# Optimization experiments

Hardware: AMD Instinct MI355X
Metric: run time of the kernel (lower is better)

## Reference

```python
import jax, jax.numpy as jnp
import numpy as np


def setup_inputs() -> dict:
    key = jax.random.key(0)
    k1, k2 = jax.random.split(key)
    B, N, M, D = 8, 8192, 8192, 3
    gts = jax.random.normal(k1, (B, N, D), dtype=jnp.float32)
    preds = jax.random.normal(k2, (B, M, D), dtype=jnp.float32)
    return {"gts": gts, "preds": preds}


def reference(gts, preds):
    # Chamfer distance (pytorch3d defaults): squared L2, mean over points,
    # mean over batch, sum of both directions.
    x2 = jnp.sum(gts * gts, axis=-1)          # [B, N]
    y2 = jnp.sum(preds * preds, axis=-1)      # [B, M]
    xy = jnp.einsum('bnd,bmd->bnm', gts, preds)  # [B, N, M]
    d2 = x2[:, :, None] + y2[:, None, :] - 2.0 * xy
    d2 = jnp.maximum(d2, 0.0)  # guard tiny negative values from cancellation
    cham_x = jnp.mean(jnp.min(d2, axis=2))  # x -> nearest y, mean over N then B
    cham_y = jnp.mean(jnp.min(d2, axis=1))  # y -> nearest x, mean over M then B
    return cham_x + cham_y
```

## Files before the change

### kernel.cpp

```cpp
#include <hip/hip_runtime.h>
#include <hip/hip_bf16.h>
#include <math.h>


#define BLOCK 256
#define WAVES 4
#define QPW 64
#define NCHUNK 2

typedef short short8 __attribute__((ext_vector_type(8)));
typedef float f32x16 __attribute__((ext_vector_type(16)));

union U16S { uint4 v; short8 s; };

__device__ __forceinline__ unsigned int bf16hi(float f) {
    __hip_bfloat16 h = __float2bfloat16(f);
    return (unsigned int)*reinterpret_cast<unsigned short*>(&h);
}
__device__ __forceinline__ float bf16f(unsigned int u) {
    unsigned short us = (unsigned short)u;
    __hip_bfloat16 h;
    *reinterpret_cast<unsigned short*>(&h) = us;
    return __bfloat162float(h);
}

__device__ __forceinline__ f32x16 mfma_bf16(short8 a, short8 b, f32x16 c) {
    f32x16 d;
    asm volatile("v_mfma_f32_32x32x16_bf16 %0, %1, %2, %3"
                 : "=v"(d) : "v"(a), "v"(b), "v"(c));
    return d;
}
__device__ __forceinline__ void mfma_fence4(f32x16& a, f32x16& b, f32x16& c, f32x16& d) {
    asm volatile("s_nop 7\n\ts_nop 7" : "+v"(a), "+v"(b), "+v"(c), "+v"(d));
}

__global__ void prep_kernel(const float* __restrict__ gts, const float* __restrict__ preds,
                            int nG, int nP, uint4* __restrict__ recG, uint4* __restrict__ recP,
                            float* out) {
    const int idx = blockIdx.x * blockDim.x + threadIdx.x;
    if (idx == 0) out[0] = 0.0f;
    if (idx >= nG + nP) return;
    const float* src;
    uint4* dst;
    if (idx < nG) { src = gts + 3 * (size_t)idx;          dst = recG + idx; }
    else          { src = preds + 3 * (size_t)(idx - nG); dst = recP + (idx - nG); }
    const float x = src[0], y = src[1], z = src[2];
    const float w = -0.5f * (x * x + y * y + z * z);
    const unsigned int xh = bf16hi(x), yh = bf16hi(y), zh = bf16hi(z), wh = bf16hi(w);
    const unsigned int xl = bf16hi(x - bf16f(xh));
    const unsigned int yl = bf16hi(y - bf16f(yh));
    const unsigned int zl = bf16hi(z - bf16f(zh));
    const unsigned int wl = bf16hi(w - bf16f(wh));
    *dst = make_uint4(xh | (yh << 16), zh | (wh << 16),
                      xl | (yl << 16), zl | (wl << 16));
}

__global__ void __launch_bounds__(BLOCK, 4)
nn_kernel(const uint4* __restrict__ recG, const uint4* __restrict__ recP,
          float* __restrict__ kpart, int N, int M, int B) {
    const int z = blockIdx.z;
    const bool dirX = (z < B);
    const int b = dirX ? z : z - B;
    const int NQ = dirX ? N : M;
    const int NR = dirX ? M : N;
    const uint4* Qr = (dirX ? recG : recP) + (size_t)b * NQ;
    const uint4* Rr = (dirX ? recP : recG) + (size_t)b * NR;
    const int nGP = B * (N + M) / 2 * 2;
    float* outK = kpart + (size_t)blockIdx.y * nGP + (dirX ? 0 : B * N) + (size_t)b * NQ;

    const int tid = threadIdx.x;
    const int lane = tid & 63;
    const int wave = tid >> 6;
    const int m = lane & 31;
    const bool hiK = lane >= 32;
    const unsigned int loMask = hiK ? 0u : 0xFFFFFFFFu;
    const int qBase = (blockIdx.x * WAVES + wave) * QPW;

    const uint4 q0 = Qr[qBase + m];
    const uint4 q1 = Qr[qBase + 32 + m];
    U16S a;
    a.v.x = q0.x;
    a.v.y = (q0.y & 0xFFFFu) | 0x3F800000u;
    a.v.z = q0.z & loMask;
    a.v.w = q0.w & 0xFFFFu & loMask;
    const short8 A0 = a.s;
    a.v.x = q1.x;
    a.v.y = (q1.y & 0xFFFFu) | 0x3F800000u;
    a.v.z = q1.z & loMask;
    a.v.w = q1.w & 0xFFFFu & loMask;
    const short8 A1 = a.s;

    f32x16 zc;
    #pragma unroll
    for (int r = 0; r < 16; ++r) zc[r] = 0.0f;
    f32x16 k0, k1;
    #pragma unroll
    for (int r = 0; r < 16; ++r) { k0[r] = -INFINITY; k1[r] = -INFINITY; }

    const int chunk = NR / NCHUNK;
    const uint2* p = (const uint2*)(Rr + (size_t)blockIdx.y * chunk) + 2 * m + (hiK ? 1 : 0);
    const int iters = chunk / 64;

    uint2 t0 = p[0], t1 = p[64];
    #pragma unroll 1
    for (int it = 0; it < iters; ++it) {
        const uint2 n0 = p[128];
        const uint2 n1 = p[192];

        U16S b0, b1;
        b0.v.x = t0.x;          b0.v.y = t0.y;
        b0.v.z = t0.x & loMask; b0.v.w = t0.y & loMask;
        b1.v.x = t1.x;          b1.v.y = t1.y;
        b1.v.z = t1.x & loMask; b1.v.w = t1.y & loMask;

        f32x16 c0 = mfma_bf16(A0, b0.s, zc);
        f32x16 c1 = mfma_bf16(A1, b0.s, zc);
        f32x16 c2 = mfma_bf16(A0, b1.s, zc);
        f32x16 c3 = mfma_bf16(A1, b1.s, zc);
        mfma_fence4(c0, c1, c2, c3);
        #pragma unroll
        for (int r = 0; r < 16; ++r) {
            k0[r] = fmaxf(fmaxf(c0[r], c2[r]), k0[r]);
            k1[r] = fmaxf(fmaxf(c1[r], c3[r]), k1[r]);
        }

        t0 = n0; t1 = n1;
        p += 128;
    }

    __shared__ float sT[WAVES][64][36];
    #pragma unroll
    for (int r = 0; r < 16; ++r) {
        const int row = (r & 3) + 8 * (r >> 2) + 4 * (lane >> 5);
        sT[wave][row][m]      = k0[r];
        sT[wave][32 + row][m] = k1[r];
    }
    const float4* rowp = (const float4*)&sT[wave][lane][0];
    float4 m01 = rowp[0];
    #pragma unroll
    for (int kk = 1; kk < 8; ++kk) {
        const float4 t = rowp[kk];
        m01.x = fmaxf(m01.x, t.x); m01.y = fmaxf(m01.y, t.y);
        m01.z = fmaxf(m01.z, t.z); m01.w = fmaxf(m01.w, t.w);
    }
    const float cmax = fmaxf(fmaxf(m01.x, m01.y), fmaxf(m01.z, m01.w));
    outK[qBase + lane] = cmax;
}

__global__ void __launch_bounds__(BLOCK)
reduce_kernel(const float* __restrict__ kpart, const float* __restrict__ gts, int nG,
              const float* __restrict__ preds, int nP,
              float invx, float invy, float* __restrict__ out) {
    const int total = nG + nP;
    float local = 0.0f;
    for (int idx = blockIdx.x * blockDim.x + threadIdx.x; idx < total;
         idx += gridDim.x * blockDim.x) {
        const float c = fmaxf(kpart[idx], kpart[total + idx]);
        const float* q;
        float inv;
        if (idx < nG) { q = gts + 3 * (size_t)idx;          inv = invx; }
        else          { q = preds + 3 * (size_t)(idx - nG); inv = invy; }
        const float q2 = q[0] * q[0] + q[1] * q[1] + q[2] * q[2];
        local += fmaxf(q2 - 2.0f * c, 0.0f) * inv;
    }
    __shared__ float waveSums[BLOCK / 64];
    float v = local;
    #pragma unroll
    for (int off = 32; off; off >>= 1) v += __shfl_xor(v, off);
    if ((threadIdx.x & 63) == 0) waveSums[threadIdx.x >> 6] = v;
    __syncthreads();
    if (threadIdx.x == 0) {
        float s = 0.0f;
        #pragma unroll
        for (int w = 0; w < BLOCK / 64; ++w) s += waveSums[w];
        atomicAdd(out, s);
    }
}

extern "C" void kernel_launch(void* const* d_in, const int* in_sizes, int n_in,
                              void* d_out, int out_size, void* d_ws, size_t ws_size,
                              hipStream_t stream) {
    const float* gts   = (const float*)d_in[0];
    const float* preds = (const float*)d_in[1];
    float* out = (float*)d_out;

    const int B = 8;
    const int N = in_sizes[0] / (B * 3);
    const int M = in_sizes[1] / (B * 3);
    const int nG = B * N, nP = B * M;

    uint4* recG  = (uint4*)d_ws;
    uint4* recP  = recG + nG;
    float* kpart = (float*)(recP + nP);

    prep_kernel<<<(nG + nP + BLOCK - 1) / BLOCK, BLOCK, 0, stream>>>(
        gts, preds, nG, nP, recG, recP, out);

    dim3 grid(N / (WAVES * QPW), NCHUNK, 2 * B);
    nn_kernel<<<grid, BLOCK, 0, stream>>>(recG, recP, kpart, N, M, B);

    reduce_kernel<<<256, BLOCK, 0, stream>>>(
        kpart, gts, nG, preds, nP, 1.0f / (float)nG, 1.0f / (float)nP, out);
}
```

Measured before the change: 97.74 us.

## Stage reference points into LDS via async global_load_lds with double buffering

The reference points are now copied into shared memory in double-buffered stages of 1024 points using direct global-to-LDS loads. The inner loop reads its operands from LDS instead of global memory. To allow plain contiguous copies, prep writes an extra pre-swizzled copy of the reference records plus precomputed squared norms, and reduce reads those norms. The MFMA/max sequence is split into two halves with shorter fences so the max work overlaps the remaining MFMA. The cost is extra workspace, extra prep writes, and a __syncthreads per stage.

```diff
diff --git a/kernel.cpp b/kernel.cpp
--- a/kernel.cpp
+++ b/kernel.cpp
@@ -7,9 +7,15 @@
 #define WAVES 4
 #define QPW 64
 #define NCHUNK 2
+#define SREF 1024
+#define STAGE_BYTES (SREF * 16)
+#define IPS (SREF / 64)
 
 typedef short short8 __attribute__((ext_vector_type(8)));
 typedef float f32x16 __attribute__((ext_vector_type(16)));
+typedef unsigned int u32;
+typedef __attribute__((address_space(1))) const u32 gu32;
+typedef __attribute__((address_space(3))) u32 lu32;
 
 union U16S { uint4 v; short8 s; };
 
@@ -30,42 +36,62 @@
                  : "=v"(d) : "v"(a), "v"(b), "v"(c));
     return d;
 }
-__device__ __forceinline__ void mfma_fence4(f32x16& a, f32x16& b, f32x16& c, f32x16& d) {
-    asm volatile("s_nop 7\n\ts_nop 7" : "+v"(a), "+v"(b), "+v"(c), "+v"(d));
+__device__ __forceinline__ void mfma_fence3(f32x16& a, f32x16& b, f32x16& c) {
+    asm volatile("s_nop 7\n\ts_nop 7" : "+v"(a), "+v"(b), "+v"(c));
+}
+__device__ __forceinline__ void mfma_fence2(f32x16& a, f32x16& b) {
+    asm volatile("s_nop 7\n\ts_nop 7\n\ts_nop 7" : "+v"(a), "+v"(b));
+}
+
+__device__ __forceinline__ void gload_lds16(const void* g, void* l) {
+    __builtin_amdgcn_global_load_lds((gu32*)g, (lu32*)l, 16, 0, 0);
 }
 
 __global__ void prep_kernel(const float* __restrict__ gts, const float* __restrict__ preds,
-                            int nG, int nP, uint4* __restrict__ recG, uint4* __restrict__ recP,
+                            int nG, int nP, uint4* __restrict__ recQ,
+                            unsigned char* __restrict__ recB, float* __restrict__ q2,
                             float* out) {
     const int idx = blockIdx.x * blockDim.x + threadIdx.x;
     if (idx == 0) out[0] = 0.0f;
     if (idx >= nG + nP) return;
     const float* src;
-    uint4* dst;
-    if (idx < nG) { src = gts + 3 * (size_t)idx;          dst = recG + idx; }
-    else          { src = preds + 3 * (size_t)(idx - nG); dst = recP + (idx - nG); }
+    unsigned char* rb;
+    if (idx < nG) {
+        src = gts + 3 * (size_t)idx;
+        rb  = recB + (size_t)(idx >> 5) * 512 + (size_t)(idx & 31) * 8;
+    } else {
+        const int j = idx - nG;
+        src = preds + 3 * (size_t)j;
+        rb  = recB + (size_t)nG * 16 + (size_t)(j >> 5) * 512 + (size_t)(j & 31) * 8;
+    }
     const float x = src[0], y = src[1], z = src[2];
-    const float w = -0.5f * (x * x + y * y + z * z);
+    const float n2 = x * x + y * y + z * z;
+    const float w = -0.5f * n2;
+    q2[idx] = n2;
     const unsigned int xh = bf16hi(x), yh = bf16hi(y), zh = bf16hi(z), wh = bf16hi(w);
     const unsigned int xl = bf16hi(x - bf16f(xh));
     const unsigned int yl = bf16hi(y - bf16f(yh));
     const unsigned int zl = bf16hi(z - bf16f(zh));
     const unsigned int wl = bf16hi(w - bf16f(wh));
-    *dst = make_uint4(xh | (yh << 16), zh | (wh << 16),
-                      xl | (yl << 16), zl | (wl << 16));
+    recQ[idx] = make_uint4(xh | (yh << 16), zh | (wh << 16),
+                           xl | (yl << 16), zl | (wl << 16));
+    *(uint2*)(rb)       = make_uint2(xh | (yh << 16), zh | (wh << 16));
+    *(uint2*)(rb + 256) = make_uint2(xl | (yl << 16), zl | (wl << 16));
 }
 
 __global__ void __launch_bounds__(BLOCK, 4)
-nn_kernel(const uint4* __restrict__ recG, const uint4* __restrict__ recP,
+nn_kernel(const uint4* __restrict__ recQ, const unsigned char* __restrict__ recB,
           float* __restrict__ kpart, int N, int M, int B) {
     const int z = blockIdx.z;
     const bool dirX = (z < B);
     const int b = dirX ? z : z - B;
     const int NQ = dirX ? N : M;
     const int NR = dirX ? M : N;
-    const uint4* Qr = (dirX ? recG : recP) + (size_t)b * NQ;
-    const uint4* Rr = (dirX ? recP : recG) + (size_t)b * NR;
-    const int nGP = B * (N + M) / 2 * 2;
+    const uint4* Qr = recQ + (dirX ? 0 : (size_t)B * N) + (size_t)b * NQ;
+    const int chunk = NR / NCHUNK;
+    const unsigned char* Rb = recB + (dirX ? (size_t)B * N * 16 : 0)
+                              + ((size_t)b * NR + (size_t)blockIdx.y * chunk) * 16;
+    const int nGP = B * (N + M);
     float* outK = kpart + (size_t)blockIdx.y * nGP + (dirX ? 0 : B * N) + (size_t)b * NQ;
 
     const int tid = threadIdx.x;
@@ -97,38 +123,57 @@
     #pragma unroll
     for (int r = 0; r < 16; ++r) { k0[r] = -INFINITY; k1[r] = -INFINITY; }
 
-    const int chunk = NR / NCHUNK;
-    const uint2* p = (const uint2*)(Rr + (size_t)blockIdx.y * chunk) + 2 * m + (hiK ? 1 : 0);
-    const int iters = chunk / 64;
-
-    uint2 t0 = p[0], t1 = p[64];
+    __shared__ __align__(16) unsigned char smem[WAVES * 64 * 36 * 4];
+
+    const unsigned char* gsrc = Rb + (size_t)wave * 4096 + (size_t)lane * 16;
+    unsigned char* lbase = smem + wave * 4096;
+    auto stage_issue = [&](int s) {
+        const unsigned char* g = gsrc + (size_t)s * STAGE_BYTES;
+        unsigned char* l = lbase + ((s & 1) * STAGE_BYTES);
+        #pragma unroll
+        for (int k2 = 0; k2 < 4; ++k2)
+            gload_lds16(g + k2 * 1024, l + k2 * 1024);
+    };
+
+    const int nStages = chunk / SREF;
+    stage_issue(0);
+    __syncthreads();
+
     #pragma unroll 1
-    for (int it = 0; it < iters; ++it) {
-        const uint2 n0 = p[128];
-        const uint2 n1 = p[192];
-
-        U16S b0, b1;
-        b0.v.x = t0.x;          b0.v.y = t0.y;
-        b0.v.z = t0.x & loMask; b0.v.w = t0.y & loMask;
-        b1.v.x = t1.x;          b1.v.y = t1.y;
-        b1.v.z = t1.x & loMask; b1.v.w = t1.y & loMask;
-
-        f32x16 c0 = mfma_bf16(A0, b0.s, zc);
-        f32x16 c1 = mfma_bf16(A1, b0.s, zc);
-        f32x16 c2 = mfma_bf16(A0, b1.s, zc);
-        f32x16 c3 = mfma_bf16(A1, b1.s, zc);
-        mfma_fence4(c0, c1, c2, c3);
+    for (int s = 0; s < nStages; ++s) {
+        if (s + 1 < nStages) stage_issue(s + 1);
+        const uint2* tp = (const uint2*)(smem + ((s & 1) * STAGE_BYTES)) + lane;
+        uint2 t0 = tp[0], t1 = tp[64];
         #pragma unroll
-        for (int r = 0; r < 16; ++r) {
-            k0[r] = fmaxf(fmaxf(c0[r], c2[r]), k0[r]);
-            k1[r] = fmaxf(fmaxf(c1[r], c3[r]), k1[r]);
+        for (int i = 0; i < IPS; ++i) {
+            uint2 n0 = t0, n1 = t1;
+            if (i + 1 < IPS) { n0 = tp[(i + 1) * 128]; n1 = tp[(i + 1) * 128 + 64]; }
+
+            U16S b0, b1;
+            b0.v.x = t0.x;          b0.v.y = t0.y;
+            b0.v.z = t0.x & loMask; b0.v.w = t0.y & loMask;
+            b1.v.x = t1.x;          b1.v.y = t1.y;
+            b1.v.z = t1.x & loMask; b1.v.w = t1.y & loMask;
+
+            f32x16 c0 = mfma_bf16(A0, b0.s, zc);
+            f32x16 c1 = mfma_bf16(A0, b1.s, zc);
+            f32x16 c2 = mfma_bf16(A1, b0.s, zc);
+            mfma_fence3(c0, c1, c2);
+            #pragma unroll
+            for (int r = 0; r < 16; ++r)
+                k0[r] = fmaxf(fmaxf(c0[r], c1[r]), k0[r]);
+            f32x16 c3 = mfma_bf16(A1, b1.s, zc);
+            mfma_fence2(c2, c3);
+            #pragma unroll
+            for (int r = 0; r < 16; ++r)
+                k1[r] = fmaxf(fmaxf(c2[r], c3[r]), k1[r]);
+
+            t0 = n0; t1 = n1;
         }
-
-        t0 = n0; t1 = n1;
-        p += 128;
-    }
-
-    __shared__ float sT[WAVES][64][36];
+        __syncthreads();
+    }
+
+    float (*sT)[64][36] = (float (*)[64][36])smem;
     #pragma unroll
     for (int r = 0; r < 16; ++r) {
         const int row = (r & 3) + 8 * (r >> 2) + 4 * (lane >> 5);
@@ -148,20 +193,15 @@
 }
 
 __global__ void __launch_bounds__(BLOCK)
-reduce_kernel(const float* __restrict__ kpart, const float* __restrict__ gts, int nG,
-              const float* __restrict__ preds, int nP,
-              float invx, float invy, float* __restrict__ out) {
+reduce_kernel(const float* __restrict__ kpart, const float* __restrict__ q2,
+              int nG, int nP, float invx, float invy, float* __restrict__ out) {
     const int total = nG + nP;
     float local = 0.0f;
     for (int idx = blockIdx.x * blockDim.x + threadIdx.x; idx < total;
          idx += gridDim.x * blockDim.x) {
         const float c = fmaxf(kpart[idx], kpart[total + idx]);
-        const float* q;
-        float inv;
-        if (idx < nG) { q = gts + 3 * (size_t)idx;          inv = invx; }
-        else          { q = preds + 3 * (size_t)(idx - nG); inv = invy; }
-        const float q2 = q[0] * q[0] + q[1] * q[1] + q[2] * q[2];
-        local += fmaxf(q2 - 2.0f * c, 0.0f) * inv;
+        const float inv = (idx < nG) ? invx : invy;
+        local += fmaxf(q2[idx] - 2.0f * c, 0.0f) * inv;
     }
     __shared__ float waveSums[BLOCK / 64];
     float v = local;
@@ -189,16 +229,17 @@
     const int M = in_sizes[1] / (B * 3);
     const int nG = B * N, nP = B * M;
 
-    uint4* recG  = (uint4*)d_ws;
-    uint4* recP  = recG + nG;
-    float* kpart = (float*)(recP + nP);
+    uint4* recQ = (uint4*)d_ws;
+    unsigned char* recB = (unsigned char*)(recQ + nG + nP);
+    float* kpart = (float*)(recB + (size_t)(nG + nP) * 16);
+    float* q2    = kpart + (size_t)NCHUNK * (nG + nP);
 
     prep_kernel<<<(nG + nP + BLOCK - 1) / BLOCK, BLOCK, 0, stream>>>(
-        gts, preds, nG, nP, recG, recP, out);
+        gts, preds, nG, nP, recQ, recB, q2, out);
 
     dim3 grid(N / (WAVES * QPW), NCHUNK, 2 * B);
-    nn_kernel<<<grid, BLOCK, 0, stream>>>(recG, recP, kpart, N, M, B);
+    nn_kernel<<<grid, BLOCK, 0, stream>>>(recQ, recB, kpart, N, M, B);
 
     reduce_kernel<<<256, BLOCK, 0, stream>>>(
-        kpart, gts, nG, preds, nP, 1.0f / (float)nG, 1.0f / (float)nP, out);
-}
+        kpart, q2, nG, nP, 1.0f / (float)nG, 1.0f / (float)nP, out);
+}
```

Result: no change. 98.79 us (+1.1%).
